# Kernel optimization log

Measured on AMD Instinct MI355X. Metric: run time of the kernel, lower is better.

Reference implementation:

```python
import jax, jax.numpy as jnp
import numpy as np

B, C, H, W = 2, 256, 128, 128
O = 256          # out_channels
KH = KW = 3
K = KH * KW      # 9 kernel taps
PAD, DIL = 1, 1


def setup_inputs() -> dict:
    key = jax.random.key(0)
    k1, k2, k3, k4, k5 = jax.random.split(key, 5)
    x = jax.random.normal(k1, (B, C, H, W), dtype=jnp.float32)
    # offset/mask predicting conv: 3*groups*K = 27 output channels.
    # scaled small so predicted offsets are O(1) pixels (torch inits these to 0).
    w_off = jax.random.normal(k2, (3 * K, C, KH, KW), dtype=jnp.float32) * 0.01
    b_off = jax.random.normal(k3, (3 * K,), dtype=jnp.float32) * 0.01
    # main weight is 1x1, later tiled to 3x3 (weight.repeat([1,1,3,3]))
    stdv = 1.0 / np.sqrt(C * KH * KW)
    weight = jax.random.uniform(k4, (O, C, 1, 1), dtype=jnp.float32, minval=-stdv, maxval=stdv)
    bias = jax.random.normal(k5, (O,), dtype=jnp.float32) * 0.01
    return {"x": x, "w_off": w_off, "b_off": b_off, "weight": weight, "bias": bias}


def _bilinear_gather(img, py, px):
    # img: [C,H,W]; py/px: [K,H,W] float sample coords. Zero outside bounds.
    y0 = jnp.floor(py).astype(jnp.int32)
    x0 = jnp.floor(px).astype(jnp.int32)
    ly = py - y0
    lx = px - x0

    def corner(yc, xc):
        valid = (yc >= 0) & (yc < H) & (xc >= 0) & (xc < W)
        v = img[:, jnp.clip(yc, 0, H - 1), jnp.clip(xc, 0, W - 1)]  # [C,K,H,W]
        return jnp.where(valid[None], v, 0.0)

    return (corner(y0, x0) * ((1 - ly) * (1 - lx))[None]
            + corner(y0, x0 + 1) * ((1 - ly) * lx)[None]
            + corner(y0 + 1, x0) * (ly * (1 - lx))[None]
            + corner(y0 + 1, x0 + 1) * (ly * lx)[None])


def reference(x, w_off, b_off, weight, bias):
    # --- offset/mask prediction conv (3x3, pad 1) ---
    tmp = jax.lax.conv_general_dilated(
        x, w_off, window_strides=(1, 1), padding=((PAD, PAD), (PAD, PAD)),
        rhs_dilation=(DIL, DIL), dimension_numbers=("NCHW", "OIHW", "NCHW"))
    tmp = tmp + b_off[None, :, None, None]
    o1, o2, mask = tmp[:, :K], tmp[:, K:2 * K], tmp[:, 2 * K:]
    offset = jnp.concatenate([o1, o2], axis=1)          # [B, 2K, H, W]
    dy = offset[:, 0::2]                                # [B, K, H, W]
    dx = offset[:, 1::2]
    # softmax over the SPATIAL axis per mask channel (as in the source)
    mask = jax.nn.softmax(mask.reshape(B, K, H * W), axis=2).reshape(B, K, H, W)

    # --- sampling grid ---
    kk = jnp.arange(K)
    ki = (kk // KW).astype(jnp.float32)
    kj = (kk % KW).astype(jnp.float32)
    base_y = ki[:, None, None] * DIL - PAD + jnp.arange(H, dtype=jnp.float32)[None, :, None]
    base_x = kj[:, None, None] * DIL - PAD + jnp.arange(W, dtype=jnp.float32)[None, None, :]
    py = dy + base_y[None]                              # [B, K, H, W]
    px = dx + base_x[None]

    sampled = jax.vmap(_bilinear_gather)(x, py, px)     # [B, C, K, H, W]
    sampled = sampled * mask[:, None]                   # modulated

    # weight.repeat([1,1,3,3]) -> same 1x1 weight at every tap
    Wk = jnp.tile(weight, (1, 1, KH, KW)).reshape(O, C, K)
    out = jnp.einsum("bckhw,ock->bohw", sampled, Wk) + bias[None, :, None, None]
    return out
```

## Files before the change

kernel.cpp:

```cpp
#include <hip/hip_runtime.h>
#include <hip/hip_fp16.h>

#define Bx 2
#define Cx 256
#define Hx 128
#define Wx 128
#define HWx (Hx*Wx)
#define Ox 256
#define Kx 9
#define NOFF 27
#define KK 2304

typedef __attribute__((ext_vector_type(8))) _Float16 f16x8;
typedef __attribute__((ext_vector_type(4))) float f32x4;


__device__ __forceinline__ unsigned short f2h(float f) {
    return __half_as_ushort(__float2half_rn(f));
}

__global__ __launch_bounds__(256) void k_pt(
        const float* __restrict__ x, const float* __restrict__ w_off,
        const float* __restrict__ weight,
        unsigned short* __restrict__ xtb, unsigned short* __restrict__ wb,
        unsigned short* __restrict__ wq) {
    if (blockIdx.x >= 2048) {
        int i = (blockIdx.x - 2048) * 256 + threadIdx.x;
        if (i < 32 * KK) {
            int oc = i / KK;
            int k  = i - oc * KK;
            int tap = k >> 8;
            int c   = k & 255;
            float v = (oc < NOFF) ? w_off[(oc * Cx + c) * 9 + tap] : 0.f;
            wb[i] = f2h(v);
        } else {
            int j = i - 32 * KK;
            if (j < Ox * Cx) wq[j] = f2h(weight[j]);
        }
        return;
    }
    __shared__ float tl[64][65];
    int tid = threadIdx.x;
    int t   = blockIdx.x;
    int b   = t >> 10;
    int r2  = t & 1023;
    int hw0 = (r2 >> 2) * 64;
    int c0  = (r2 & 3) * 64;
#pragma unroll
    for (int r = 0; r < 4; r++) {
        int cl = r * 16 + (tid >> 4);
        int hl = (tid & 15) * 4;
        const float4 v = *(const float4*)&x[((size_t)(b * Cx + c0 + cl)) * HWx + hw0 + hl];
        tl[cl][hl + 0] = v.x; tl[cl][hl + 1] = v.y; tl[cl][hl + 2] = v.z; tl[cl][hl + 3] = v.w;
    }
    __syncthreads();
#pragma unroll
    for (int r = 0; r < 4; r++) {
        int hl = r * 16 + (tid >> 4);
        int cl = (tid & 15) * 4;
        ushort4 o;
        o.x = f2h(tl[cl + 0][hl]); o.y = f2h(tl[cl + 1][hl]);
        o.z = f2h(tl[cl + 2][hl]); o.w = f2h(tl[cl + 3][hl]);
        *(ushort4*)&xtb[((size_t)b * HWx + hw0 + hl) * Cx + c0 + cl] = o;
    }
}

__global__ __launch_bounds__(256) void k1_mfma(
        const unsigned short* __restrict__ xtb, const unsigned short* __restrict__ wb,
        const float* __restrict__ b_off, float* __restrict__ tmp_t,
        float* __restrict__ pscr) {
    int band = blockIdx.x & 7;
    int idx  = blockIdx.x >> 3;
    int y    = band * 16 + (idx >> 2);
    int qt   = idx & 3;
    int px0  = qt * 32;
    int b    = blockIdx.y;

    __shared__ unsigned short As[102 * 72];
    __shared__ float wmx[2][9], wsum[2][9];
    int tid  = threadIdx.x;
    int wave = tid >> 6, lane = tid & 63;
    int quad = lane >> 4, col = lane & 15;
    int wmh  = wave >> 1;
    int wn   = wave & 1;

    f32x4 acc = {};
    const unsigned short* xb = xtb + (size_t)b * HWx * Cx;

#pragma unroll 1
    for (int ph = 0; ph < 4; ph++) {
        __syncthreads();
        for (int u = tid; u < 816; u += 256) {
            int slot = u >> 3;
            int ci   = (u & 7) * 8;
            int r = (slot >= 68) ? 2 : (slot >= 34 ? 1 : 0);
            int p = slot - r * 34;
            int yy = y + r - 1;
            int px = px0 + p - 1;
            uint4 v = make_uint4(0u, 0u, 0u, 0u);
            if (yy >= 0 && yy < Hx && px >= 0 && px < Wx)
                v = *(const uint4*)(xb + ((size_t)(yy * Wx + px)) * Cx + ph * 64 + ci);
            *(uint4*)&As[slot * 72 + ci] = v;
        }
        __syncthreads();
#pragma unroll
        for (int r = 0; r < 3; r++)
#pragma unroll
        for (int dc = 0; dc < 3; dc++)
#pragma unroll
        for (int s = 0; s < 2; s++) {
            int kl  = s * 32 + quad * 8;
            int kg  = (r * 3 + dc) * 256 + ph * 64 + kl;
            int base = r * 34 + dc;
            f16x8 a0 = *(const f16x8*)&As[(base + wmh * 16 + col) * 72 + kl];
            f16x8 b0 = *(const f16x8*)(wb + (size_t)(wn * 16 + col) * KK + kg);
            acc = __builtin_amdgcn_mfma_f32_16x16x32_f16(a0, b0, acc, 0, 0, 0);
        }
    }

    float* orow = tmp_t + ((size_t)(b * HWx) + (size_t)y * Wx + px0) * 32;
    int oc = wn * 16 + col;
    float bo = (oc < NOFF) ? b_off[oc] : 0.f;
#pragma unroll
    for (int r4 = 0; r4 < 4; r4++) {
        int pxd = wmh * 16 + quad * 4 + r4;
        float v = acc[r4] + bo;
        acc[r4] = v;
        orow[(size_t)pxd * 32 + oc] = v;
    }

    float m4 = fmaxf(fmaxf(acc[0], acc[1]), fmaxf(acc[2], acc[3]));
    m4 = fmaxf(m4, __shfl_xor(m4, 16));
    m4 = fmaxf(m4, __shfl_xor(m4, 32));
    float s4 = __expf(acc[0] - m4) + __expf(acc[1] - m4)
             + __expf(acc[2] - m4) + __expf(acc[3] - m4);
    s4 += __shfl_xor(s4, 16);
    s4 += __shfl_xor(s4, 32);
    if (wn == 1 && quad == 0 && col >= 2 && col <= 10) {
        wmx[wmh][col - 2] = m4;
        wsum[wmh][col - 2] = s4;
    }
    __syncthreads();
    if (tid < 9) {
        float M = fmaxf(wmx[0][tid], wmx[1][tid]);
        float S = wsum[0][tid] * __expf(wmx[0][tid] - M)
                + wsum[1][tid] * __expf(wmx[1][tid] - M);
        int blkid = y * 4 + qt;
        int pidx  = (b * 512 + blkid) * 9 + tid;
        pscr[pidx] = M;
        pscr[9216 + pidx] = S;
    }
}

__global__ void k2b(const float* __restrict__ pscr, float* __restrict__ stats) {
    int bk = blockIdx.x;
    int b = bk / Kx, k = bk % Kx;
    int s = threadIdx.x;
    int idx = (b * 512 + s) * 9 + k;
    float m = pscr[idx];
    float p = pscr[9216 + idx];
    float M = m;
    for (int off = 32; off > 0; off >>= 1) M = fmaxf(M, __shfl_xor(M, off));
    float e = p * __expf(m - M);
    for (int off = 32; off > 0; off >>= 1) e += __shfl_xor(e, off);
    __shared__ float sm[8], ss[8];
    int wave = s >> 6, lane = s & 63;
    if (lane == 0) { sm[wave] = M; ss[wave] = e; }
    __syncthreads();
    if (s == 0) {
        float Mf = sm[0];
#pragma unroll
        for (int i = 1; i < 8; i++) Mf = fmaxf(Mf, sm[i]);
        float S = 0.f;
#pragma unroll
        for (int i = 0; i < 8; i++) S += ss[i] * __expf(sm[i] - Mf);
        stats[bk * 2] = Mf;
        stats[bk * 2 + 1] = 1.f / S;
    }
}

__global__ __launch_bounds__(256) void k35_fused(
        const unsigned short* __restrict__ xtb, const float* __restrict__ tmp_t,
        const float* __restrict__ stats, const unsigned short* __restrict__ wq,
        const float* __restrict__ bias, float* __restrict__ out) {
    __shared__ __half2 lwh[64][36];
    __shared__ int     lo[64][36];
    __shared__ unsigned short As[64][264];
    int tid  = threadIdx.x;
    int band = blockIdx.x & 7;
    int sub  = blockIdx.x >> 3;
    int b    = blockIdx.y;
    int px0  = (band * 32 + sub) * 64;

    for (int u = tid; u < 576; u += 256) {
        int px = u / 9, k = u - px * 9;
        int hw = px0 + px;
        int y  = hw >> 7;
        int xx = hw & (Wx - 1);
        const float* trow = tmp_t + ((size_t)b * HWx + hw) * 32;
        float dy = trow[2 * k];
        float dx = trow[2 * k + 1];
        float lg = trow[18 + k];
        float m  = __expf(lg - stats[(b * Kx + k) * 2]) * stats[(b * Kx + k) * 2 + 1] * 256.f;
        float py = dy + (float)(k / 3 - 1 + y);
        float px_ = dx + (float)(k % 3 - 1 + xx);
        float fy = floorf(py), fx = floorf(px_);
        int y0 = (int)fy, x0 = (int)fx;
        float ly = py - fy, lx = px_ - fx;
        float w00 = (1.f - ly) * (1.f - lx) * m;
        float w01 = (1.f - ly) * lx * m;
        float w10 = ly * (1.f - lx) * m;
        float w11 = ly * lx * m;
        int y1 = y0 + 1, x1 = x0 + 1;
        bool vy0 = (y0 >= 0) & (y0 < Hx), vy1 = (y1 >= 0) & (y1 < Hx);
        bool vx0 = (x0 >= 0) & (x0 < Wx), vx1 = (x1 >= 0) & (x1 < Wx);
        int cy0 = min(max(y0, 0), Hx - 1), cy1 = min(max(y1, 0), Hx - 1);
        int cx0 = min(max(x0, 0), Wx - 1), cx1 = min(max(x1, 0), Wx - 1);
        float a00 = (vy0 && vx0) ? w00 : 0.f;
        float a01 = (vy0 && vx1) ? w01 : 0.f;
        float a10 = (vy1 && vx0) ? w10 : 0.f;
        float a11 = (vy1 && vx1) ? w11 : 0.f;
        lwh[px][4 * k + 0] = __half2half2(__float2half_rn(a00));  lo[px][4 * k + 0] = cy0 * Wx + cx0;
        lwh[px][4 * k + 1] = __half2half2(__float2half_rn(a01));  lo[px][4 * k + 1] = cy0 * Wx + cx1;
        lwh[px][4 * k + 2] = __half2half2(__float2half_rn(a10));  lo[px][4 * k + 2] = cy1 * Wx + cx0;
        lwh[px][4 * k + 3] = __half2half2(__float2half_rn(a11));  lo[px][4 * k + 3] = cy1 * Wx + cx1;
    }
    __syncthreads();

    int wave = tid >> 6;
    int lane = tid & 63;
    int half = lane >> 5;
    int li   = lane & 31;
    const unsigned short* xb = xtb + (size_t)b * HWx * Cx + li * 8;
    const __half2 uns = __half2half2(__float2half_rn(1.f / 256.f));
#pragma unroll 1
    for (int pass = 0; pass < 8; pass++) {
        int px = wave * 16 + pass * 2 + half;
        __half2 a0 = __half2half2(__ushort_as_half(0));
        __half2 a1 = a0, a2 = a0, a3 = a0;
#pragma unroll
        for (int j = 0; j < 36; j++) {
            __half2 w = lwh[px][j];
            int   off = lo[px][j];
            uint4 v = *(const uint4*)(xb + (size_t)off * Cx);
            a0 = __hfma2(w, *(__half2*)&v.x, a0);
            a1 = __hfma2(w, *(__half2*)&v.y, a1);
            a2 = __hfma2(w, *(__half2*)&v.z, a2);
            a3 = __hfma2(w, *(__half2*)&v.w, a3);
        }
        a0 = __hmul2(a0, uns); a1 = __hmul2(a1, uns);
        a2 = __hmul2(a2, uns); a3 = __hmul2(a3, uns);
        uint4 r;
        r.x = *(unsigned*)&a0; r.y = *(unsigned*)&a1;
        r.z = *(unsigned*)&a2; r.w = *(unsigned*)&a3;
        *(uint4*)&As[px][li * 8] = r;
    }
    __syncthreads();

    int quad = lane >> 4, col = lane & 15;
    f32x4 acc[4][4] = {};
#pragma unroll
    for (int ki = 0; ki < 8; ki++) {
        int k0 = ki * 32;
        f16x8 a[4], w[4];
#pragma unroll
        for (int mt = 0; mt < 4; mt++)
            a[mt] = *(const f16x8*)&As[mt * 16 + col][k0 + quad * 8];
#pragma unroll
        for (int nt = 0; nt < 4; nt++)
            w[nt] = *(const f16x8*)(wq + (size_t)(wave * 64 + nt * 16 + col) * Cx + k0 + quad * 8);
#pragma unroll
        for (int mt = 0; mt < 4; mt++)
#pragma unroll
            for (int nt = 0; nt < 4; nt++)
                acc[mt][nt] = __builtin_amdgcn_mfma_f32_16x16x32_f16(a[mt], w[nt], acc[mt][nt], 0, 0, 0);
    }

#pragma unroll
    for (int nt = 0; nt < 4; nt++) {
        int oc = wave * 64 + nt * 16 + col;
        float bo = bias[oc];
#pragma unroll
        for (int mt = 0; mt < 4; mt++) {
            int hw = px0 + mt * 16 + quad * 4;
            float4 v;
            v.x = acc[mt][nt][0] + bo; v.y = acc[mt][nt][1] + bo;
            v.z = acc[mt][nt][2] + bo; v.w = acc[mt][nt][3] + bo;
            *(float4*)&out[((size_t)(b * Ox + oc)) * HWx + hw] = v;
        }
    }
}

extern "C" void kernel_launch(void* const* d_in, const int* in_sizes, int n_in,
                              void* d_out, int out_size, void* d_ws, size_t ws_size,
                              hipStream_t stream) {
    const float*    x      = (const float*)d_in[0];
    const float*    w_off  = (const float*)d_in[1];
    const float*    b_off  = (const float*)d_in[2];
    const float*    weight = (const float*)d_in[3];
    const float*    bias   = (const float*)d_in[4];
    float* out = (float*)d_out;
    float* ws  = (float*)d_ws;

    float*          tmp_t = ws;
    float*          stats = ws + 1048576;
    unsigned short* wbq   = (unsigned short*)(ws + 1048640);
    unsigned short* xtb   = (unsigned short*)(ws + 1085504);
    unsigned short* wq    = (unsigned short*)(ws + 5279808);
    float*          pscr  = (float*)d_out;

    k_pt<<<dim3(2592), 256, 0, stream>>>(x, w_off, weight, xtb, wbq, wq);
    k1_mfma<<<dim3(512, Bx), 256, 0, stream>>>(xtb, wbq, b_off, tmp_t, pscr);
    k2b<<<dim3(Bx * Kx), 512, 0, stream>>>(pscr, stats);
    k35_fused<<<dim3(256, Bx), 256, 0, stream>>>(xtb, tmp_t, stats, wq, bias, out);
}
```

Baseline: 164.2 us.

## Double-buffer offset-conv LDS tiles and fold softmax stats reduction into sampling kernel

The offset-prediction conv kernel now double-buffers its LDS input tile, prefetching the next channel phase into registers while the current phase runs on MFMA. It also hoists the weight fragments into registers and pads the LDS row stride from 72 to 80. The separate spatial-softmax statistics kernel is removed. Each block of the fused sampling kernel now redundantly reduces the per-block partial max/sum scratch, which has been relaid out contiguously per (batch, tap) and moved into the workspace. This saves a launch and a dependency at the cost of duplicated reduction work and more LDS.

```diff
diff --git a/kernel.cpp b/kernel.cpp
--- a/kernel.cpp
+++ b/kernel.cpp
@@ -10,6 +10,10 @@
 #define Kx 9
 #define NOFF 27
 #define KK 2304
+
+#define SLOT 80
+#define NSLOT 102
+#define ABUF (NSLOT*SLOT)
 
 typedef __attribute__((ext_vector_type(8))) _Float16 f16x8;
 typedef __attribute__((ext_vector_type(4))) float f32x4;
@@ -76,7 +80,7 @@
     int px0  = qt * 32;
     int b    = blockIdx.y;
 
-    __shared__ unsigned short As[102 * 72];
+    __shared__ unsigned short As[2 * ABUF];
     __shared__ float wmx[2][9], wsum[2][9];
     int tid  = threadIdx.x;
     int wave = tid >> 6, lane = tid & 63;
@@ -84,38 +88,74 @@
     int wmh  = wave >> 1;
     int wn   = wave & 1;
 
+    const unsigned short* xb = xtb + (size_t)b * HWx * Cx;
+    const unsigned short* sp[4];
+    int  sdst[4];
+    bool sstp[4], sldp[4];
+#pragma unroll
+    for (int i = 0; i < 4; i++) {
+        int u = tid + i * 256;
+        bool uv = (u < 816);
+        int slot = u >> 3;
+        int ci   = (u & 7) * 8;
+        int r = (slot >= 68) ? 2 : (slot >= 34 ? 1 : 0);
+        int p = slot - r * 34;
+        int yy = y + r - 1;
+        int px = px0 + p - 1;
+        bool ib = uv && (yy >= 0) && (yy < Hx) && (px >= 0) && (px < Wx);
+        int lin = ib ? (yy * Wx + px) : 0;
+        sp[i]   = xb + (size_t)lin * Cx + ci;
+        sdst[i] = slot * SLOT + ci;
+        sstp[i] = uv;
+        sldp[i] = ib;
+    }
+
     f32x4 acc = {};
-    const unsigned short* xb = xtb + (size_t)b * HWx * Cx;
+    const unsigned short* wrow = wb + (size_t)(wn * 16 + col) * KK;
+    int abase = (wmh * 16 + col) * SLOT + quad * 8;
+
+    {
+        uint4 sreg[4];
+#pragma unroll
+        for (int i = 0; i < 4; i++)
+            sreg[i] = sldp[i] ? *(const uint4*)(sp[i]) : make_uint4(0u, 0u, 0u, 0u);
+#pragma unroll
+        for (int i = 0; i < 4; i++)
+            if (sstp[i]) *(uint4*)&As[sdst[i]] = sreg[i];
+    }
+    __syncthreads();
 
 #pragma unroll 1
     for (int ph = 0; ph < 4; ph++) {
+        const unsigned short* Ab = As + (ph & 1) * ABUF;
+        unsigned short*       Aw = As + ((ph & 1) ^ 1) * ABUF;
+        uint4 sreg[4];
+        if (ph < 3) {
+#pragma unroll
+            for (int i = 0; i < 4; i++)
+                sreg[i] = sldp[i] ? *(const uint4*)(sp[i] + (ph + 1) * 64)
+                                  : make_uint4(0u, 0u, 0u, 0u);
+        }
+#pragma unroll
+        for (int s = 0; s < 2; s++) {
+            f16x8 breg[9];
+#pragma unroll
+            for (int t = 0; t < 9; t++)
+                breg[t] = *(const f16x8*)(wrow + t * 256 + ph * 64 + s * 32 + quad * 8);
+#pragma unroll
+            for (int r = 0; r < 3; r++)
+#pragma unroll
+            for (int dc = 0; dc < 3; dc++) {
+                f16x8 a0 = *(const f16x8*)&Ab[(r * 34 + dc) * SLOT + abase + s * 32];
+                acc = __builtin_amdgcn_mfma_f32_16x16x32_f16(a0, breg[r * 3 + dc], acc, 0, 0, 0);
+            }
+        }
+        if (ph < 3) {
+#pragma unroll
+            for (int i = 0; i < 4; i++)
+                if (sstp[i]) *(uint4*)&Aw[sdst[i]] = sreg[i];
+        }
         __syncthreads();
-        for (int u = tid; u < 816; u += 256) {
-            int slot = u >> 3;
-            int ci   = (u & 7) * 8;
-            int r = (slot >= 68) ? 2 : (slot >= 34 ? 1 : 0);
-            int p = slot - r * 34;
-            int yy = y + r - 1;
-            int px = px0 + p - 1;
-            uint4 v = make_uint4(0u, 0u, 0u, 0u);
-            if (yy >= 0 && yy < Hx && px >= 0 && px < Wx)
-                v = *(const uint4*)(xb + ((size_t)(yy * Wx + px)) * Cx + ph * 64 + ci);
-            *(uint4*)&As[slot * 72 + ci] = v;
-        }
-        __syncthreads();
-#pragma unroll
-        for (int r = 0; r < 3; r++)
-#pragma unroll
-        for (int dc = 0; dc < 3; dc++)
-#pragma unroll
-        for (int s = 0; s < 2; s++) {
-            int kl  = s * 32 + quad * 8;
-            int kg  = (r * 3 + dc) * 256 + ph * 64 + kl;
-            int base = r * 34 + dc;
-            f16x8 a0 = *(const f16x8*)&As[(base + wmh * 16 + col) * 72 + kl];
-            f16x8 b0 = *(const f16x8*)(wb + (size_t)(wn * 16 + col) * KK + kg);
-            acc = __builtin_amdgcn_mfma_f32_16x16x32_f16(a0, b0, acc, 0, 0, 0);
-        }
     }
 
     float* orow = tmp_t + ((size_t)(b * HWx) + (size_t)y * Wx + px0) * 32;
@@ -146,51 +186,58 @@
         float S = wsum[0][tid] * __expf(wmx[0][tid] - M)
                 + wsum[1][tid] * __expf(wmx[1][tid] - M);
         int blkid = y * 4 + qt;
-        int pidx  = (b * 512 + blkid) * 9 + tid;
+        int pidx  = (b * 9 + tid) * 512 + blkid;
         pscr[pidx] = M;
         pscr[9216 + pidx] = S;
     }
 }
 
-__global__ void k2b(const float* __restrict__ pscr, float* __restrict__ stats) {
-    int bk = blockIdx.x;
-    int b = bk / Kx, k = bk % Kx;
-    int s = threadIdx.x;
-    int idx = (b * 512 + s) * 9 + k;
-    float m = pscr[idx];
-    float p = pscr[9216 + idx];
-    float M = m;
-    for (int off = 32; off > 0; off >>= 1) M = fmaxf(M, __shfl_xor(M, off));
-    float e = p * __expf(m - M);
-    for (int off = 32; off > 0; off >>= 1) e += __shfl_xor(e, off);
-    __shared__ float sm[8], ss[8];
-    int wave = s >> 6, lane = s & 63;
-    if (lane == 0) { sm[wave] = M; ss[wave] = e; }
-    __syncthreads();
-    if (s == 0) {
-        float Mf = sm[0];
-#pragma unroll
-        for (int i = 1; i < 8; i++) Mf = fmaxf(Mf, sm[i]);
-        float S = 0.f;
-#pragma unroll
-        for (int i = 0; i < 8; i++) S += ss[i] * __expf(sm[i] - Mf);
-        stats[bk * 2] = Mf;
-        stats[bk * 2 + 1] = 1.f / S;
-    }
-}
-
 __global__ __launch_bounds__(256) void k35_fused(
         const unsigned short* __restrict__ xtb, const float* __restrict__ tmp_t,
-        const float* __restrict__ stats, const unsigned short* __restrict__ wq,
+        const float* __restrict__ pscr, const unsigned short* __restrict__ wq,
         const float* __restrict__ bias, float* __restrict__ out) {
     __shared__ __half2 lwh[64][36];
     __shared__ int     lo[64][36];
     __shared__ unsigned short As[64][264];
+    __shared__ float sst9[9][2];
+    __shared__ float xm[4][9], xe[4][9];
     int tid  = threadIdx.x;
     int band = blockIdx.x & 7;
     int sub  = blockIdx.x >> 3;
     int b    = blockIdx.y;
     int px0  = (band * 32 + sub) * 64;
+
+    {
+        int wv = tid >> 6, ln = tid & 63;
+        int s0 = tid * 2;
+#pragma unroll 1
+        for (int g = 0; g < 9; g++) {
+            const float* pm = pscr + (size_t)(b * 9 + g) * 512;
+            float m0 = pm[s0], m1 = pm[s0 + 1];
+            float e0 = pm[9216 + s0], e1 = pm[9216 + s0 + 1];
+            float M = fmaxf(m0, m1);
+            float E = e0 * __expf(m0 - M) + e1 * __expf(m1 - M);
+            for (int off = 32; off > 0; off >>= 1) {
+                float Mo = __shfl_xor(M, off);
+                float Eo = __shfl_xor(E, off);
+                float Mn = fmaxf(M, Mo);
+                E = E * __expf(M - Mn) + Eo * __expf(Mo - Mn);
+                M = Mn;
+            }
+            if (ln == 0) { xm[wv][g] = M; xe[wv][g] = E; }
+        }
+    }
+    __syncthreads();
+    if (tid < 9) {
+        float Mf = fmaxf(fmaxf(xm[0][tid], xm[1][tid]), fmaxf(xm[2][tid], xm[3][tid]));
+        float S = xe[0][tid] * __expf(xm[0][tid] - Mf)
+                + xe[1][tid] * __expf(xm[1][tid] - Mf)
+                + xe[2][tid] * __expf(xm[2][tid] - Mf)
+                + xe[3][tid] * __expf(xm[3][tid] - Mf);
+        sst9[tid][0] = Mf;
+        sst9[tid][1] = 1.f / S;
+    }
+    __syncthreads();
 
     for (int u = tid; u < 576; u += 256) {
         int px = u / 9, k = u - px * 9;
@@ -201,7 +248,7 @@
         float dy = trow[2 * k];
         float dx = trow[2 * k + 1];
         float lg = trow[18 + k];
-        float m  = __expf(lg - stats[(b * Kx + k) * 2]) * stats[(b * Kx + k) * 2 + 1] * 256.f;
+        float m  = __expf(lg - sst9[k][0]) * sst9[k][1] * 256.f;
         float py = dy + (float)(k / 3 - 1 + y);
         float px_ = dx + (float)(k % 3 - 1 + xx);
         float fy = floorf(py), fx = floorf(px_);
@@ -303,14 +350,12 @@
     float* ws  = (float*)d_ws;
 
     float*          tmp_t = ws;
-    float*          stats = ws + 1048576;
     unsigned short* wbq   = (unsigned short*)(ws + 1048640);
     unsigned short* xtb   = (unsigned short*)(ws + 1085504);
     unsigned short* wq    = (unsigned short*)(ws + 5279808);
-    float*          pscr  = (float*)d_out;
+    float*          pscr  = ws + 5312576;
 
     k_pt<<<dim3(2592), 256, 0, stream>>>(x, w_off, weight, xtb, wbq, wq);
     k1_mfma<<<dim3(512, Bx), 256, 0, stream>>>(xtb, wbq, b_off, tmp_t, pscr);
-    k2b<<<dim3(Bx * Kx), 512, 0, stream>>>(pscr, stats);
-    k35_fused<<<dim3(256, Bx), 256, 0, stream>>>(xtb, tmp_t, stats, wq, bias, out);
-}
+    k35_fused<<<dim3(256, Bx), 256, 0, stream>>>(xtb, tmp_t, pscr, wq, bias, out);
+}
```

After: 166.4 us. No clear change (+1.3%).
